# Kernel tuning notes

Measured on AMD Instinct MI355X. Metric: run time of the kernel, lower is better.

The kernel has to match this reference:

```python
import jax, jax.numpy as jnp
import numpy as np

N = 8192       # nodes
F_IN = 512     # input features
H = 8          # heads (layer 1)
C1 = 8         # per-head channels (layer 1)
NC = 16        # num classes
E = 262144     # edges (avg degree 32)
NEG_SLOPE = 0.2


def setup_inputs() -> dict:
    key = jax.random.key(0)
    ks = jax.random.split(key, 11)
    s = 0.1
    return {
        "x": jax.random.normal(ks[0], (N, F_IN), jnp.float32),
        "edge_index": jax.random.randint(ks[1], (2, E), 0, N, dtype=jnp.int32),
        "W1": jax.random.normal(ks[2], (F_IN, H * C1), jnp.float32) * s,
        "a_src1": jax.random.normal(ks[3], (H, C1), jnp.float32) * s,
        "a_dst1": jax.random.normal(ks[4], (H, C1), jnp.float32) * s,
        "b1": jnp.zeros((H * C1,), jnp.float32),
        "W2": jax.random.normal(ks[5], (H * C1, NC), jnp.float32) * s,
        "a_src2": jax.random.normal(ks[6], (1, NC), jnp.float32) * s,
        "a_dst2": jax.random.normal(ks[7], (1, NC), jnp.float32) * s,
        "b2": jnp.zeros((NC,), jnp.float32),
    }


def _gat_layer(x, W, a_src, a_dst, b, src, dst, heads, outc, concat):
    n = x.shape[0]
    h = (x @ W).reshape(n, heads, outc)                      # [N,H,C]
    al_s = jnp.einsum('nhc,hc->nh', h, a_src)                 # [N,H]
    al_d = jnp.einsum('nhc,hc->nh', h, a_dst)                 # [N,H]
    e = jax.nn.leaky_relu(al_s[src] + al_d[dst], NEG_SLOPE)   # [E,H]
    # segment softmax over destination node (every node has a self-loop)
    m = jax.ops.segment_max(e, dst, num_segments=n)
    ex = jnp.exp(e - m[dst])
    denom = jax.ops.segment_sum(ex, dst, num_segments=n)
    alpha = ex / denom[dst]                                   # [E,H]
    out = jax.ops.segment_sum(alpha[:, :, None] * h[src], dst, num_segments=n)  # [N,H,C]
    out = out.reshape(n, heads * outc) if concat else out.mean(axis=1)
    return out + b


def reference(x, edge_index, W1, a_src1, a_dst1, b1, W2, a_src2, a_dst2, b2):
    # add self-loops (PyG GATConv default)
    loop = jnp.arange(N, dtype=edge_index.dtype)
    src = jnp.concatenate([edge_index[0], loop])
    dst = jnp.concatenate([edge_index[1], loop])
    # dropout layers are identity in eval mode
    h1 = jax.nn.elu(_gat_layer(x, W1, a_src1, a_dst1, b1, src, dst, H, C1, True))
    z = _gat_layer(h1, W2, a_src2, a_dst2, b2, src, dst, 1, NC, False)
    return jax.nn.log_softmax(z, axis=-1), z @ z.T
```

## Files before the change

kernel.cpp:

```cpp
#include <hip/hip_runtime.h>
#include <math.h>

#define N_NODES 8192
#define F_IN 512
#define NH1 8
#define C1 8
#define D1 64
#define NC 16
#define E_EDGES 262144
#define TOT_EDGES (E_EDGES + N_NODES)
#define NEG_SLOPE 0.2f
#define CAP 128

__global__ __launch_bounds__(256) void gemm1_k(const float* __restrict__ x,
                                               const float* __restrict__ W1,
                                               const float* __restrict__ a_src1,
                                               const float* __restrict__ a_dst1,
                                               float* __restrict__ h1pre,
                                               float* __restrict__ als1,
                                               float* __restrict__ ald1) {
    __shared__ __align__(16) float As[32 * 34];
    __shared__ __align__(16) float Bs[32 * 68];
    int tid = threadIdx.x;
    int rowBase = blockIdx.x * 32;
    int rm = tid >> 4, rn = tid & 15;
    float acc[2][4] = {};
    for (int k0 = 0; k0 < F_IN; k0 += 32) {
#pragma unroll
        for (int j = 0; j < 4; ++j) {
            int i = tid + 256 * j;
            int r = i >> 5, c = i & 31;
            As[c * 34 + r] = x[(rowBase + r) * F_IN + k0 + c];
        }
#pragma unroll
        for (int j = 0; j < 8; ++j) {
            int i = tid + 256 * j;
            int rr = i >> 6, cc = i & 63;
            Bs[rr * 68 + cc] = W1[(k0 + rr) * D1 + cc];
        }
        __syncthreads();
#pragma unroll
        for (int kk = 0; kk < 32; ++kk) {
            float2 a = *(const float2*)&As[kk * 34 + rm * 2];
            float4 b = *(const float4*)&Bs[kk * 68 + rn * 4];
            float av[2] = {a.x, a.y};
            float bv[4] = {b.x, b.y, b.z, b.w};
#pragma unroll
            for (int jj = 0; jj < 2; ++jj)
#pragma unroll
                for (int ll = 0; ll < 4; ++ll)
                    acc[jj][ll] = fmaf(av[jj], bv[ll], acc[jj][ll]);
        }
        __syncthreads();
    }
    int h = rn >> 1, half = rn & 1;
#pragma unroll
    for (int jj = 0; jj < 2; ++jj) {
        int row = rowBase + rm * 2 + jj;
        float4 o = {acc[jj][0], acc[jj][1], acc[jj][2], acc[jj][3]};
        *(float4*)&h1pre[(size_t)row * D1 + rn * 4] = o;
        float ps = 0.f, pd = 0.f;
#pragma unroll
        for (int ll = 0; ll < 4; ++ll) {
            ps = fmaf(acc[jj][ll], a_src1[h * C1 + half * 4 + ll], ps);
            pd = fmaf(acc[jj][ll], a_dst1[h * C1 + half * 4 + ll], pd);
        }
        ps += __shfl_xor(ps, 1);
        pd += __shfl_xor(pd, 1);
        if (half == 0) {
            als1[row * NH1 + h] = ps;
            ald1[row * NH1 + h] = pd;
        }
    }
}

__global__ void hist_k(const int* __restrict__ ei, int* __restrict__ counts) {
    int i = blockIdx.x * blockDim.x + threadIdx.x;
    if (i >= TOT_EDGES) return;
    int dst = (i < E_EDGES) ? ei[E_EDGES + i] : (i - E_EDGES);
    atomicAdd(&counts[dst], 1);
}

__global__ __launch_bounds__(1024) void scan_k(const int* __restrict__ counts,
                                               int* __restrict__ offsets, int* __restrict__ cursor) {
    __shared__ int wtot[16];
    __shared__ int wbase[16];
    int t = threadIdx.x;
    int lane = t & 63, wid = t >> 6;
    int local[8];
    int s = 0;
#pragma unroll
    for (int j = 0; j < 8; ++j) { local[j] = counts[t * 8 + j]; s += local[j]; }
    int incl = s;
#pragma unroll
    for (int d = 1; d < 64; d <<= 1) {
        int v = __shfl_up(incl, d);
        if (lane >= d) incl += v;
    }
    if (lane == 63) wtot[wid] = incl;
    __syncthreads();
    if (t < 16) {
        int v = wtot[t];
        int iv = v;
#pragma unroll
        for (int d = 1; d < 16; d <<= 1) {
            int u = __shfl_up(iv, d);
            if (t >= d) iv += u;
        }
        wbase[t] = iv - v;
    }
    __syncthreads();
    int run = wbase[wid] + incl - s;
#pragma unroll
    for (int j = 0; j < 8; ++j) {
        offsets[t * 8 + j] = run;
        cursor[t * 8 + j] = run;
        run += local[j];
    }
    if (t == 1023) offsets[8192] = run;
}

__global__ void scatter_k(const int* __restrict__ ei, int* __restrict__ cursor, int* __restrict__ csr) {
    int i = blockIdx.x * blockDim.x + threadIdx.x;
    if (i >= TOT_EDGES) return;
    int src, dst;
    if (i < E_EDGES) { src = ei[i]; dst = ei[E_EDGES + i]; }
    else             { src = i - E_EDGES; dst = src; }
    int pos = atomicAdd(&cursor[dst], 1);
    csr[pos] = src;
}

__global__ __launch_bounds__(64) void agg1_k(const float* __restrict__ h1pre,
                                             const float* __restrict__ als1, const float* __restrict__ ald1,
                                             const int* __restrict__ offsets, const int* __restrict__ csr,
                                             const float* __restrict__ b1,
                                             const float* __restrict__ W2,
                                             const float* __restrict__ a_src2, const float* __restrict__ a_dst2,
                                             float* __restrict__ h2pre,
                                             float* __restrict__ als2, float* __restrict__ ald2) {
    __shared__ int   csr_s[CAP];
    __shared__ float vbuf[CAP * NH1];
    __shared__ float vals[64];
    int n = blockIdx.x, t = threadIdx.x;
    int beg = offsets[n], end = offsets[n + 1];
    int deg = end - beg;
    float val;
    if (deg <= CAP) {
        int h = t & 7, eo = t >> 3;
        float aldh = ald1[n * NH1 + h];
        float m = -3.4e38f;
        for (int e = eo; e < deg; e += 8) {
            int s = csr[beg + e];
            if (h == 0) csr_s[e] = s;
            float v = als1[s * NH1 + h] + aldh;
            v = v > 0.f ? v : NEG_SLOPE * v;
            vbuf[e * NH1 + h] = v;
            m = fmaxf(m, v);
        }
        m = fmaxf(m, __shfl_xor(m, 8));
        m = fmaxf(m, __shfl_xor(m, 16));
        m = fmaxf(m, __shfl_xor(m, 32));
        float den = 0.f;
        for (int e = eo; e < deg; e += 8) {
            float w = expf(vbuf[e * NH1 + h] - m);
            vbuf[e * NH1 + h] = w;
            den += w;
        }
        den += __shfl_xor(den, 8);
        den += __shfl_xor(den, 16);
        den += __shfl_xor(den, 32);
        __syncthreads();
        int q = t >> 3;
        float dq = __shfl(den, q);
        float acc = 0.f;
        int e = 0;
        for (; e + 4 <= deg; e += 4) {
            int s0 = csr_s[e], s1 = csr_s[e + 1], s2 = csr_s[e + 2], s3 = csr_s[e + 3];
            float w0 = vbuf[e * NH1 + q], w1 = vbuf[(e + 1) * NH1 + q];
            float w2 = vbuf[(e + 2) * NH1 + q], w3 = vbuf[(e + 3) * NH1 + q];
            acc = fmaf(w0, h1pre[s0 * D1 + t], acc);
            acc = fmaf(w1, h1pre[s1 * D1 + t], acc);
            acc = fmaf(w2, h1pre[s2 * D1 + t], acc);
            acc = fmaf(w3, h1pre[s3 * D1 + t], acc);
        }
        for (; e < deg; ++e)
            acc = fmaf(vbuf[e * NH1 + q], h1pre[csr_s[e] * D1 + t], acc);
        val = acc / dq + b1[t];
    } else {
        int h = t & 7;
        float aldh = ald1[n * NH1 + h];
        float m = -3.4e38f;
        for (int i = beg + (t >> 3); i < end; i += 8) {
            int s = csr[i];
            float v = als1[s * NH1 + h] + aldh;
            v = v > 0.f ? v : NEG_SLOPE * v;
            m = fmaxf(m, v);
        }
        m = fmaxf(m, __shfl_xor(m, 8));
        m = fmaxf(m, __shfl_xor(m, 16));
        m = fmaxf(m, __shfl_xor(m, 32));
        float den = 0.f;
        for (int i = beg + (t >> 3); i < end; i += 8) {
            int s = csr[i];
            float v = als1[s * NH1 + h] + aldh;
            v = v > 0.f ? v : NEG_SLOPE * v;
            den += expf(v - m);
        }
        den += __shfl_xor(den, 8);
        den += __shfl_xor(den, 16);
        den += __shfl_xor(den, 32);
        int q = t >> 3;
        float mq = __shfl(m, q);
        float dq = __shfl(den, q);
        float aldq = ald1[n * NH1 + q];
        float acc = 0.f;
        for (int i = beg; i < end; ++i) {
            int s = csr[i];
            float v = als1[s * NH1 + q] + aldq;
            v = v > 0.f ? v : NEG_SLOPE * v;
            acc = fmaf(expf(v - mq), h1pre[s * D1 + t], acc);
        }
        val = acc / dq + b1[t];
    }
    val = val > 0.f ? val : expm1f(val);
    __syncthreads();
    vals[t] = val;
    __syncthreads();
    int g = t >> 4, c = t & 15;
    float a2 = 0.f;
    const float* w2p = W2 + g * 16 * NC + c;
#pragma unroll
    for (int j = 0; j < 16; ++j)
        a2 = fmaf(vals[g * 16 + j], w2p[j * NC], a2);
    a2 += __shfl_xor(a2, 16);
    a2 += __shfl_xor(a2, 32);
    if (t < 16) h2pre[(size_t)n * NC + t] = a2;
    float ps = a2 * a_src2[c], pd = a2 * a_dst2[c];
#pragma unroll
    for (int d = 1; d < 16; d <<= 1) {
        ps += __shfl_xor(ps, d);
        pd += __shfl_xor(pd, d);
    }
    if (t == 0) { als2[n] = ps; ald2[n] = pd; }
}

__global__ __launch_bounds__(64) void agg2_k(const float* __restrict__ h2pre,
                                             const float* __restrict__ als2, const float* __restrict__ ald2,
                                             const int* __restrict__ offsets, const int* __restrict__ csr,
                                             const float* __restrict__ b2,
                                             float* __restrict__ z, float* __restrict__ out_ls) {
    __shared__ int   csr2[CAP];
    __shared__ float wb2[CAP];
    int n = blockIdx.x, t = threadIdx.x;
    int beg = offsets[n], end = offsets[n + 1];
    int deg = end - beg;
    float aldn = ald2[n];
    int eg = t >> 4, c = t & 15;
    float zv;
    if (deg <= CAP) {
        float m = -3.4e38f;
        for (int i = t; i < deg; i += 64) {
            int s = csr[beg + i];
            csr2[i] = s;
            float v = als2[s] + aldn;
            v = v > 0.f ? v : NEG_SLOPE * v;
            wb2[i] = v;
            m = fmaxf(m, v);
        }
#pragma unroll
        for (int d = 1; d < 64; d <<= 1) m = fmaxf(m, __shfl_xor(m, d));
        float den = 0.f;
        for (int i = t; i < deg; i += 64) {
            float w = expf(wb2[i] - m);
            wb2[i] = w;
            den += w;
        }
#pragma unroll
        for (int d = 1; d < 64; d <<= 1) den += __shfl_xor(den, d);
        __syncthreads();
        float acc = 0.f;
        int e = eg;
        for (; e + 4 < deg; e += 8) {
            int s0 = csr2[e], s1 = csr2[e + 4];
            float w0 = wb2[e], w1 = wb2[e + 4];
            acc = fmaf(w0, h2pre[s0 * NC + c], acc);
            acc = fmaf(w1, h2pre[s1 * NC + c], acc);
        }
        for (; e < deg; e += 4)
            acc = fmaf(wb2[e], h2pre[csr2[e] * NC + c], acc);
        acc += __shfl_xor(acc, 16);
        acc += __shfl_xor(acc, 32);
        zv = acc / den + b2[c];
    } else {
        float m = -3.4e38f;
        for (int i = beg + t; i < end; i += 64) {
            float v = als2[csr[i]] + aldn;
            v = v > 0.f ? v : NEG_SLOPE * v;
            m = fmaxf(m, v);
        }
#pragma unroll
        for (int d = 1; d < 64; d <<= 1) m = fmaxf(m, __shfl_xor(m, d));
        float den = 0.f;
        for (int i = beg + t; i < end; i += 64) {
            float v = als2[csr[i]] + aldn;
            v = v > 0.f ? v : NEG_SLOPE * v;
            den += expf(v - m);
        }
#pragma unroll
        for (int d = 1; d < 64; d <<= 1) den += __shfl_xor(den, d);
        float acc = 0.f;
        for (int i = beg + eg; i < end; i += 4) {
            int s = csr[i];
            float v = als2[s] + aldn;
            v = v > 0.f ? v : NEG_SLOPE * v;
            acc = fmaf(expf(v - m), h2pre[(size_t)s * NC + c], acc);
        }
        acc += __shfl_xor(acc, 16);
        acc += __shfl_xor(acc, 32);
        zv = acc / den + b2[c];
    }
    if (t < 16) z[(size_t)n * NC + t] = zv;
    float zm = zv;
#pragma unroll
    for (int d = 1; d < 16; d <<= 1) zm = fmaxf(zm, __shfl_xor(zm, d));
    float se = expf(zv - zm);
#pragma unroll
    for (int d = 1; d < 16; d <<= 1) se += __shfl_xor(se, d);
    if (t < 16) out_ls[(size_t)n * NC + t] = zv - (zm + logf(se));
}

__global__ __launch_bounds__(256) void gram_k(const float* __restrict__ z,
                                              float* __restrict__ out) {
    __shared__ __align__(16) float rz[64 * 16];
    int tid = threadIdx.x;
    int colBase = blockIdx.x * 256;
    int rowBase = blockIdx.y * 64;
    ((float4*)rz)[tid] = ((const float4*)z)[rowBase * 4 + tid];
    int j = colBase + tid;
    float c[16];
#pragma unroll
    for (int k4 = 0; k4 < 4; ++k4) {
        float4 v = ((const float4*)(z + (size_t)j * 16))[k4];
        c[k4 * 4 + 0] = v.x; c[k4 * 4 + 1] = v.y; c[k4 * 4 + 2] = v.z; c[k4 * 4 + 3] = v.w;
    }
    __syncthreads();
#pragma unroll 4
    for (int r = 0; r < 64; ++r) {
        const float* zr = &rz[r * 16];
        float acc = 0.f;
#pragma unroll
        for (int k = 0; k < 16; ++k) acc = fmaf(c[k], zr[k], acc);
        out[(size_t)(rowBase + r) * N_NODES + j] = acc;
    }
}

extern "C" void kernel_launch(void* const* d_in, const int* in_sizes, int n_in,
                              void* d_out, int out_size, void* d_ws, size_t ws_size,
                              hipStream_t stream) {
    (void)in_sizes; (void)n_in; (void)out_size; (void)ws_size;
    const float* x      = (const float*)d_in[0];
    const int*   ei     = (const int*)d_in[1];
    const float* W1     = (const float*)d_in[2];
    const float* a_src1 = (const float*)d_in[3];
    const float* a_dst1 = (const float*)d_in[4];
    const float* b1     = (const float*)d_in[5];
    const float* W2     = (const float*)d_in[6];
    const float* a_src2 = (const float*)d_in[7];
    const float* a_dst2 = (const float*)d_in[8];
    const float* b2     = (const float*)d_in[9];
    float* out = (float*)d_out;

    char* ws = (char*)d_ws;
    float* h1pre  = (float*)(ws + 0);
    float* als1   = (float*)(ws + 4194304);
    float* ald1   = (float*)(ws + 4456448);
    float* h2pre  = (float*)(ws + 4718592);
    float* als2   = (float*)(ws + 5242880);
    float* ald2   = (float*)(ws + 5275648);
    float* zarr   = (float*)(ws + 5308416);
    int*   counts = (int*)  (ws + 5832704);
    int*   offsets= (int*)  (ws + 5865472);
    int*   cursor = (int*)  (ws + 5898496);
    int*   csr    = (int*)  (ws + 5931264);

    hipMemsetAsync(counts, 0, N_NODES * sizeof(int), stream);
    hist_k<<<(TOT_EDGES + 255) / 256, 256, 0, stream>>>(ei, counts);
    scan_k<<<1, 1024, 0, stream>>>(counts, offsets, cursor);
    scatter_k<<<(TOT_EDGES + 255) / 256, 256, 0, stream>>>(ei, cursor, csr);

    gemm1_k<<<N_NODES / 32, 256, 0, stream>>>(x, W1, a_src1, a_dst1, h1pre, als1, ald1);
    agg1_k<<<N_NODES, 64, 0, stream>>>(h1pre, als1, ald1, offsets, csr, b1,
                                       W2, a_src2, a_dst2, h2pre, als2, ald2);
    agg2_k<<<N_NODES, 64, 0, stream>>>(h2pre, als2, ald2, offsets, csr, b2, zarr, out);

    gram_k<<<dim3(N_NODES / 256, N_NODES / 64), 256, 0, stream>>>(zarr, out + (size_t)N_NODES * NC);
}
```

Baseline: 368.3 us.

## Fuse CSR build into one cooperative kernel and fold counts zeroing into GEMM

Replaces the memset plus the separate histogram, scan and scatter kernels with a single cooperative kernel that uses grid-wide syncs between phases. Zeroing of the counts array moves into the first GEMM kernel. agg1 now stages the CSR neighbour list into shared memory cooperatively before the softmax loop. The aim is to remove several launch gaps. The trade-off is that only one block performs the scan while the rest of the grid waits, and cooperative-launch requirements could limit residency.

```diff
diff --git a/kernel.cpp b/kernel.cpp
--- a/kernel.cpp
+++ b/kernel.cpp
@@ -1,5 +1,8 @@
 #include <hip/hip_runtime.h>
+#include <hip/hip_cooperative_groups.h>
 #include <math.h>
+
+namespace cg = cooperative_groups;
 
 #define N_NODES 8192
 #define F_IN 512
@@ -18,10 +21,12 @@
                                                const float* __restrict__ a_dst1,
                                                float* __restrict__ h1pre,
                                                float* __restrict__ als1,
-                                               float* __restrict__ ald1) {
+                                               float* __restrict__ ald1,
+                                               int* __restrict__ counts) {
     __shared__ __align__(16) float As[32 * 34];
     __shared__ __align__(16) float Bs[32 * 68];
     int tid = threadIdx.x;
+    if (tid < 32) counts[blockIdx.x * 32 + tid] = 0;
     int rowBase = blockIdx.x * 32;
     int rm = tid >> 4, rn = tid & 15;
     float acc[2][4] = {};
@@ -74,60 +79,65 @@
     }
 }
 
-__global__ void hist_k(const int* __restrict__ ei, int* __restrict__ counts) {
-    int i = blockIdx.x * blockDim.x + threadIdx.x;
-    if (i >= TOT_EDGES) return;
-    int dst = (i < E_EDGES) ? ei[E_EDGES + i] : (i - E_EDGES);
-    atomicAdd(&counts[dst], 1);
-}
-
-__global__ __launch_bounds__(1024) void scan_k(const int* __restrict__ counts,
-                                               int* __restrict__ offsets, int* __restrict__ cursor) {
+__global__ __launch_bounds__(1024) void csr_coop_k(const int* __restrict__ ei,
+                                                   int* __restrict__ counts,
+                                                   int* __restrict__ offsets,
+                                                   int* __restrict__ cursor,
+                                                   int* __restrict__ csr) {
     __shared__ int wtot[16];
     __shared__ int wbase[16];
-    int t = threadIdx.x;
-    int lane = t & 63, wid = t >> 6;
-    int local[8];
-    int s = 0;
-#pragma unroll
-    for (int j = 0; j < 8; ++j) { local[j] = counts[t * 8 + j]; s += local[j]; }
-    int incl = s;
-#pragma unroll
-    for (int d = 1; d < 64; d <<= 1) {
-        int v = __shfl_up(incl, d);
-        if (lane >= d) incl += v;
-    }
-    if (lane == 63) wtot[wid] = incl;
-    __syncthreads();
-    if (t < 16) {
-        int v = wtot[t];
-        int iv = v;
-#pragma unroll
-        for (int d = 1; d < 16; d <<= 1) {
-            int u = __shfl_up(iv, d);
-            if (t >= d) iv += u;
-        }
-        wbase[t] = iv - v;
-    }
-    __syncthreads();
-    int run = wbase[wid] + incl - s;
-#pragma unroll
-    for (int j = 0; j < 8; ++j) {
-        offsets[t * 8 + j] = run;
-        cursor[t * 8 + j] = run;
-        run += local[j];
-    }
-    if (t == 1023) offsets[8192] = run;
-}
-
-__global__ void scatter_k(const int* __restrict__ ei, int* __restrict__ cursor, int* __restrict__ csr) {
-    int i = blockIdx.x * blockDim.x + threadIdx.x;
-    if (i >= TOT_EDGES) return;
-    int src, dst;
-    if (i < E_EDGES) { src = ei[i]; dst = ei[E_EDGES + i]; }
-    else             { src = i - E_EDGES; dst = src; }
-    int pos = atomicAdd(&cursor[dst], 1);
-    csr[pos] = src;
+    cg::grid_group grid = cg::this_grid();
+    int gtid = blockIdx.x * 1024 + threadIdx.x;
+    for (int i = gtid; i < TOT_EDGES; i += 256 * 1024) {
+        int dst = (i < E_EDGES) ? ei[E_EDGES + i] : (i - E_EDGES);
+        atomicAdd(&counts[dst], 1);
+    }
+    __threadfence();
+    grid.sync();
+    if (blockIdx.x == 0) {
+        int t = threadIdx.x;
+        int lane = t & 63, wid = t >> 6;
+        int local[8];
+        int s = 0;
+#pragma unroll
+        for (int j = 0; j < 8; ++j) { local[j] = counts[t * 8 + j]; s += local[j]; }
+        int incl = s;
+#pragma unroll
+        for (int d = 1; d < 64; d <<= 1) {
+            int v = __shfl_up(incl, d);
+            if (lane >= d) incl += v;
+        }
+        if (lane == 63) wtot[wid] = incl;
+        __syncthreads();
+        if (t < 16) {
+            int v = wtot[t];
+            int iv = v;
+#pragma unroll
+            for (int d = 1; d < 16; d <<= 1) {
+                int u = __shfl_up(iv, d);
+                if (t >= d) iv += u;
+            }
+            wbase[t] = iv - v;
+        }
+        __syncthreads();
+        int run = wbase[wid] + incl - s;
+#pragma unroll
+        for (int j = 0; j < 8; ++j) {
+            offsets[t * 8 + j] = run;
+            cursor[t * 8 + j] = run;
+            run += local[j];
+        }
+        if (t == 1023) offsets[8192] = run;
+    }
+    __threadfence();
+    grid.sync();
+    for (int i = gtid; i < TOT_EDGES; i += 256 * 1024) {
+        int src, dst;
+        if (i < E_EDGES) { src = ei[i]; dst = ei[E_EDGES + i]; }
+        else             { src = i - E_EDGES; dst = src; }
+        int pos = atomicAdd(&cursor[dst], 1);
+        csr[pos] = src;
+    }
 }
 
 __global__ __launch_bounds__(64) void agg1_k(const float* __restrict__ h1pre,
@@ -146,12 +156,13 @@
     int deg = end - beg;
     float val;
     if (deg <= CAP) {
+        for (int i = t; i < deg; i += 64) csr_s[i] = csr[beg + i];
+        __syncthreads();
         int h = t & 7, eo = t >> 3;
         float aldh = ald1[n * NH1 + h];
         float m = -3.4e38f;
         for (int e = eo; e < deg; e += 8) {
-            int s = csr[beg + e];
-            if (h == 0) csr_s[e] = s;
+            int s = csr_s[e];
             float v = als1[s * NH1 + h] + aldh;
             v = v > 0.f ? v : NEG_SLOPE * v;
             vbuf[e * NH1 + h] = v;
@@ -383,12 +394,13 @@
     int*   cursor = (int*)  (ws + 5898496);
     int*   csr    = (int*)  (ws + 5931264);
 
-    hipMemsetAsync(counts, 0, N_NODES * sizeof(int), stream);
-    hist_k<<<(TOT_EDGES + 255) / 256, 256, 0, stream>>>(ei, counts);
-    scan_k<<<1, 1024, 0, stream>>>(counts, offsets, cursor);
-    scatter_k<<<(TOT_EDGES + 255) / 256, 256, 0, stream>>>(ei, cursor, csr);
-
-    gemm1_k<<<N_NODES / 32, 256, 0, stream>>>(x, W1, a_src1, a_dst1, h1pre, als1, ald1);
+    gemm1_k<<<N_NODES / 32, 256, 0, stream>>>(x, W1, a_src1, a_dst1, h1pre, als1, ald1, counts);
+
+    {
+        void* cargs[] = {(void*)&ei, (void*)&counts, (void*)&offsets, (void*)&cursor, (void*)&csr};
+        hipLaunchCooperativeKernel((const void*)csr_coop_k, dim3(256), dim3(1024), cargs, 0, stream);
+    }
+
     agg1_k<<<N_NODES, 64, 0, stream>>>(h1pre, als1, ald1, offsets, csr, b1,
                                        W2, a_src2, a_dst2, h2pre, als2, ald2);
     agg2_k<<<N_NODES, 64, 0, stream>>>(h2pre, als2, ald2, offsets, csr, b2, zarr, out);
```

New measurement: 552.0 us. 49.8% more time.

## Replace CSR build with padded ELL buckets and fuse count zeroing into GEMM

Applied to the files above, without the earlier changes.

Drops the histogram, scan and scatter passes and the memset. Instead, a single kernel appends each edge's source into a fixed 128-slot bucket per destination node, using an atomic counter. Edges beyond the cap go to a small global overflow list, which the high-degree aggregation paths scan linearly. Zeroing of the counters moves into the first GEMM kernel. This removes three kernel launches and a serial single-block scan, at the cost of a padded, larger adjacency array and a slow fallback for high-degree nodes.

```diff
diff --git a/kernel.cpp b/kernel.cpp
--- a/kernel.cpp
+++ b/kernel.cpp
@@ -11,6 +11,8 @@
 #define TOT_EDGES (E_EDGES + N_NODES)
 #define NEG_SLOPE 0.2f
 #define CAP 128
+#define CAPE 128
+#define OVF_MAX 8192
 
 __global__ __launch_bounds__(256) void gemm1_k(const float* __restrict__ x,
                                                const float* __restrict__ W1,
@@ -18,10 +20,13 @@
                                                const float* __restrict__ a_dst1,
                                                float* __restrict__ h1pre,
                                                float* __restrict__ als1,
-                                               float* __restrict__ ald1) {
+                                               float* __restrict__ ald1,
+                                               int* __restrict__ counts) {
     __shared__ __align__(16) float As[32 * 34];
     __shared__ __align__(16) float Bs[32 * 68];
     int tid = threadIdx.x;
+    if (tid < 32) counts[blockIdx.x * 32 + tid] = 0;
+    if (blockIdx.x == 0 && tid == 32) counts[N_NODES] = 0;
     int rowBase = blockIdx.x * 32;
     int rm = tid >> 4, rn = tid & 15;
     float acc[2][4] = {};
@@ -74,65 +79,26 @@
     }
 }
 
-__global__ void hist_k(const int* __restrict__ ei, int* __restrict__ counts) {
-    int i = blockIdx.x * blockDim.x + threadIdx.x;
-    if (i >= TOT_EDGES) return;
-    int dst = (i < E_EDGES) ? ei[E_EDGES + i] : (i - E_EDGES);
-    atomicAdd(&counts[dst], 1);
-}
-
-__global__ __launch_bounds__(1024) void scan_k(const int* __restrict__ counts,
-                                               int* __restrict__ offsets, int* __restrict__ cursor) {
-    __shared__ int wtot[16];
-    __shared__ int wbase[16];
-    int t = threadIdx.x;
-    int lane = t & 63, wid = t >> 6;
-    int local[8];
-    int s = 0;
-#pragma unroll
-    for (int j = 0; j < 8; ++j) { local[j] = counts[t * 8 + j]; s += local[j]; }
-    int incl = s;
-#pragma unroll
-    for (int d = 1; d < 64; d <<= 1) {
-        int v = __shfl_up(incl, d);
-        if (lane >= d) incl += v;
-    }
-    if (lane == 63) wtot[wid] = incl;
-    __syncthreads();
-    if (t < 16) {
-        int v = wtot[t];
-        int iv = v;
-#pragma unroll
-        for (int d = 1; d < 16; d <<= 1) {
-            int u = __shfl_up(iv, d);
-            if (t >= d) iv += u;
-        }
-        wbase[t] = iv - v;
-    }
-    __syncthreads();
-    int run = wbase[wid] + incl - s;
-#pragma unroll
-    for (int j = 0; j < 8; ++j) {
-        offsets[t * 8 + j] = run;
-        cursor[t * 8 + j] = run;
-        run += local[j];
-    }
-    if (t == 1023) offsets[8192] = run;
-}
-
-__global__ void scatter_k(const int* __restrict__ ei, int* __restrict__ cursor, int* __restrict__ csr) {
+__global__ void ell_k(const int* __restrict__ ei, int* __restrict__ counts,
+                      int* __restrict__ ell, int* __restrict__ ovfd, int* __restrict__ ovfs) {
     int i = blockIdx.x * blockDim.x + threadIdx.x;
     if (i >= TOT_EDGES) return;
     int src, dst;
     if (i < E_EDGES) { src = ei[i]; dst = ei[E_EDGES + i]; }
     else             { src = i - E_EDGES; dst = src; }
-    int pos = atomicAdd(&cursor[dst], 1);
-    csr[pos] = src;
+    int pos = atomicAdd(&counts[dst], 1);
+    if (pos < CAPE) {
+        ell[dst * CAPE + pos] = src;
+    } else {
+        int p2 = atomicAdd(&counts[N_NODES], 1);
+        if (p2 < OVF_MAX) { ovfd[p2] = dst; ovfs[p2] = src; }
+    }
 }
 
 __global__ __launch_bounds__(64) void agg1_k(const float* __restrict__ h1pre,
                                              const float* __restrict__ als1, const float* __restrict__ ald1,
-                                             const int* __restrict__ offsets, const int* __restrict__ csr,
+                                             const int* __restrict__ counts, const int* __restrict__ ell,
+                                             const int* __restrict__ ovfd, const int* __restrict__ ovfs,
                                              const float* __restrict__ b1,
                                              const float* __restrict__ W2,
                                              const float* __restrict__ a_src2, const float* __restrict__ a_dst2,
@@ -142,16 +108,17 @@
     __shared__ float vbuf[CAP * NH1];
     __shared__ float vals[64];
     int n = blockIdx.x, t = threadIdx.x;
-    int beg = offsets[n], end = offsets[n + 1];
-    int deg = end - beg;
+    int deg = counts[n];
+    int beg = n * CAPE;
     float val;
     if (deg <= CAP) {
+        for (int i = t; i < deg; i += 64) csr_s[i] = ell[beg + i];
+        __syncthreads();
         int h = t & 7, eo = t >> 3;
         float aldh = ald1[n * NH1 + h];
         float m = -3.4e38f;
         for (int e = eo; e < deg; e += 8) {
-            int s = csr[beg + e];
-            if (h == 0) csr_s[e] = s;
+            int s = csr_s[e];
             float v = als1[s * NH1 + h] + aldh;
             v = v > 0.f ? v : NEG_SLOPE * v;
             vbuf[e * NH1 + h] = v;
@@ -187,11 +154,19 @@
             acc = fmaf(vbuf[e * NH1 + q], h1pre[csr_s[e] * D1 + t], acc);
         val = acc / dq + b1[t];
     } else {
+        int degc = deg < CAPE ? deg : CAPE;
+        int novf = counts[N_NODES]; novf = novf < OVF_MAX ? novf : OVF_MAX;
         int h = t & 7;
         float aldh = ald1[n * NH1 + h];
         float m = -3.4e38f;
-        for (int i = beg + (t >> 3); i < end; i += 8) {
-            int s = csr[i];
+        for (int i = (t >> 3); i < degc; i += 8) {
+            int s = ell[beg + i];
+            float v = als1[s * NH1 + h] + aldh;
+            v = v > 0.f ? v : NEG_SLOPE * v;
+            m = fmaxf(m, v);
+        }
+        for (int k = (t >> 3); k < novf; k += 8) if (ovfd[k] == n) {
+            int s = ovfs[k];
             float v = als1[s * NH1 + h] + aldh;
             v = v > 0.f ? v : NEG_SLOPE * v;
             m = fmaxf(m, v);
@@ -200,8 +175,14 @@
         m = fmaxf(m, __shfl_xor(m, 16));
         m = fmaxf(m, __shfl_xor(m, 32));
         float den = 0.f;
-        for (int i = beg + (t >> 3); i < end; i += 8) {
-            int s = csr[i];
+        for (int i = (t >> 3); i < degc; i += 8) {
+            int s = ell[beg + i];
+            float v = als1[s * NH1 + h] + aldh;
+            v = v > 0.f ? v : NEG_SLOPE * v;
+            den += expf(v - m);
+        }
+        for (int k = (t >> 3); k < novf; k += 8) if (ovfd[k] == n) {
+            int s = ovfs[k];
             float v = als1[s * NH1 + h] + aldh;
             v = v > 0.f ? v : NEG_SLOPE * v;
             den += expf(v - m);
@@ -214,8 +195,14 @@
         float dq = __shfl(den, q);
         float aldq = ald1[n * NH1 + q];
         float acc = 0.f;
-        for (int i = beg; i < end; ++i) {
-            int s = csr[i];
+        for (int i = 0; i < degc; ++i) {
+            int s = ell[beg + i];
+            float v = als1[s * NH1 + q] + aldq;
+            v = v > 0.f ? v : NEG_SLOPE * v;
+            acc = fmaf(expf(v - mq), h1pre[s * D1 + t], acc);
+        }
+        for (int k = 0; k < novf; ++k) if (ovfd[k] == n) {
+            int s = ovfs[k];
             float v = als1[s * NH1 + q] + aldq;
             v = v > 0.f ? v : NEG_SLOPE * v;
             acc = fmaf(expf(v - mq), h1pre[s * D1 + t], acc);
@@ -246,21 +233,22 @@
 
 __global__ __launch_bounds__(64) void agg2_k(const float* __restrict__ h2pre,
                                              const float* __restrict__ als2, const float* __restrict__ ald2,
-                                             const int* __restrict__ offsets, const int* __restrict__ csr,
+                                             const int* __restrict__ counts, const int* __restrict__ ell,
+                                             const int* __restrict__ ovfd, const int* __restrict__ ovfs,
                                              const float* __restrict__ b2,
                                              float* __restrict__ z, float* __restrict__ out_ls) {
     __shared__ int   csr2[CAP];
     __shared__ float wb2[CAP];
     int n = blockIdx.x, t = threadIdx.x;
-    int beg = offsets[n], end = offsets[n + 1];
-    int deg = end - beg;
+    int deg = counts[n];
+    int beg = n * CAPE;
     float aldn = ald2[n];
     int eg = t >> 4, c = t & 15;
     float zv;
     if (deg <= CAP) {
         float m = -3.4e38f;
         for (int i = t; i < deg; i += 64) {
-            int s = csr[beg + i];
+            int s = ell[beg + i];
             csr2[i] = s;
             float v = als2[s] + aldn;
             v = v > 0.f ? v : NEG_SLOPE * v;
@@ -292,25 +280,43 @@
         acc += __shfl_xor(acc, 32);
         zv = acc / den + b2[c];
     } else {
+        int degc = deg < CAPE ? deg : CAPE;
+        int novf = counts[N_NODES]; novf = novf < OVF_MAX ? novf : OVF_MAX;
         float m = -3.4e38f;
-        for (int i = beg + t; i < end; i += 64) {
-            float v = als2[csr[i]] + aldn;
+        for (int i = t; i < degc; i += 64) {
+            float v = als2[ell[beg + i]] + aldn;
+            v = v > 0.f ? v : NEG_SLOPE * v;
+            m = fmaxf(m, v);
+        }
+        for (int k = t; k < novf; k += 64) if (ovfd[k] == n) {
+            float v = als2[ovfs[k]] + aldn;
             v = v > 0.f ? v : NEG_SLOPE * v;
             m = fmaxf(m, v);
         }
 #pragma unroll
         for (int d = 1; d < 64; d <<= 1) m = fmaxf(m, __shfl_xor(m, d));
         float den = 0.f;
-        for (int i = beg + t; i < end; i += 64) {
-            float v = als2[csr[i]] + aldn;
+        for (int i = t; i < degc; i += 64) {
+            float v = als2[ell[beg + i]] + aldn;
             v = v > 0.f ? v : NEG_SLOPE * v;
             den += expf(v - m);
         }
+        for (int k = t; k < novf; k += 64) if (ovfd[k] == n) {
+            float v = als2[ovfs[k]] + aldn;
+            v = v > 0.f ? v : NEG_SLOPE * v;
+            den += expf(v - m);
+        }
 #pragma unroll
         for (int d = 1; d < 64; d <<= 1) den += __shfl_xor(den, d);
         float acc = 0.f;
-        for (int i = beg + eg; i < end; i += 4) {
-            int s = csr[i];
+        for (int i = eg; i < degc; i += 4) {
+            int s = ell[beg + i];
+            float v = als2[s] + aldn;
+            v = v > 0.f ? v : NEG_SLOPE * v;
+            acc = fmaf(expf(v - m), h2pre[(size_t)s * NC + c], acc);
+        }
+        for (int k = eg; k < novf; k += 4) if (ovfd[k] == n) {
+            int s = ovfs[k];
             float v = als2[s] + aldn;
             v = v > 0.f ? v : NEG_SLOPE * v;
             acc = fmaf(expf(v - m), h2pre[(size_t)s * NC + c], acc);
@@ -372,26 +378,21 @@
 
     char* ws = (char*)d_ws;
     float* h1pre  = (float*)(ws + 0);
-    float* als1   = (float*)(ws + 4194304);
-    float* ald1   = (float*)(ws + 4456448);
-    float* h2pre  = (float*)(ws + 4718592);
-    float* als2   = (float*)(ws + 5242880);
-    float* ald2   = (float*)(ws + 5275648);
-    float* zarr   = (float*)(ws + 5308416);
-    int*   counts = (int*)  (ws + 5832704);
-    int*   offsets= (int*)  (ws + 5865472);
-    int*   cursor = (int*)  (ws + 5898496);
-    int*   csr    = (int*)  (ws + 5931264);
-
-    hipMemsetAsync(counts, 0, N_NODES * sizeof(int), stream);
-    hist_k<<<(TOT_EDGES + 255) / 256, 256, 0, stream>>>(ei, counts);
-    scan_k<<<1, 1024, 0, stream>>>(counts, offsets, cursor);
-    scatter_k<<<(TOT_EDGES + 255) / 256, 256, 0, stream>>>(ei, cursor, csr);
-
-    gemm1_k<<<N_NODES / 32, 256, 0, stream>>>(x, W1, a_src1, a_dst1, h1pre, als1, ald1);
-    agg1_k<<<N_NODES, 64, 0, stream>>>(h1pre, als1, ald1, offsets, csr, b1,
+    float* als1   = (float*)(ws + 2097152);
+    float* ald1   = (float*)(ws + 2359296);
+    float* h2pre  = (float*)(ws + 2621440);
+    float* als2   = (float*)(ws + 3145728);
+    float* ald2   = (float*)(ws + 3178496);
+    float* zarr   = (float*)(ws + 3211264);
+    int*   counts = (int*)  (ws + 3735552);
+    int*   ell    = (int*)  (ws + 3768576);
+    int*   ovfd   = (int*)  (ws + 7962880);
+    int*   ovfs   = (int*)  (ws + 7995648);
+
+    gemm1_k<<<N_NODES / 32, 256, 0, stream>>>(x, W1, a_src1, a_dst1, h1pre, als1, ald1, counts);
+    ell_k<<<(TOT_EDGES + 255) / 256, 256, 0, stream>>>(ei, counts, ell, ovfd, ovfs);
+    agg1_k<<<N_NODES, 64, 0, stream>>>(h1pre, als1, ald1, counts, ell, ovfd, ovfs, b1,
                                        W2, a_src2, a_dst2, h2pre, als2, ald2);
-    agg2_k<<<N_NODES, 64, 0, stream>>>(h2pre, als2, ald2, offsets, csr, b2, zarr, out);
-
+    agg2_k<<<N_NODES, 64, 0, stream>>>(h2pre, als2, ald2, counts, ell, ovfd, ovfs, b2, zarr, out);
     gram_k<<<dim3(N_NODES / 256, N_NODES / 64), 256, 0, stream>>>(zarr, out + (size_t)N_NODES * NC);
 }
```

After: 347.1 us. -5.8%, faster.
